# Kernel optimization log

Hardware: AMD Instinct MI355X
Metric: run time of the kernel (lower is better)

## Reference

```python
import jax, jax.numpy as jnp
import numpy as np

RADIUS = 1.0  # from init_kwargs
B = 8388608

def setup_inputs() -> dict:
    key = jax.random.key(0)
    k1, k2 = jax.random.split(key)
    x = jax.random.normal(k1, (B, 3), dtype=jnp.float32)
    center = jax.random.normal(k2, (B, 3), dtype=jnp.float32)
    return {"x": x, "center": center}

def reference(x, center):
    # Closed-form solution of: min ||z - x||^2  s.t. ||z - center||^2 <= r^2
    # z = x if inside the ball, else center + r * (x - center)/||x - center||
    d = x - center                                   # [B, 3]
    n = jnp.linalg.norm(d, axis=-1, keepdims=True)   # [B, 1]
    scale = jnp.minimum(jnp.float32(1.0), RADIUS / jnp.maximum(n, jnp.float32(1e-12)))
    return center + d * scale
```

## Files before the change

### kernel.cpp

```cpp
#include <hip/hip_runtime.h>


#define RADIUS 1.0f

typedef float fvec4 __attribute__((ext_vector_type(4)));

__global__ __launch_bounds__(256) void circle_proj_ilp8(
    const fvec4* __restrict__ xv,
    const fvec4* __restrict__ cv,
    fvec4* __restrict__ ov,
    int ngroups)
{
    int t = blockIdx.x * blockDim.x + threadIdx.x;
    if (t >= ngroups) return;
    long base = (long)t * 6;

    fvec4 xr[6], cr[6];
#pragma unroll
    for (int k = 0; k < 6; ++k) xr[k] = xv[base + k];
#pragma unroll
    for (int k = 0; k < 6; ++k) cr[k] = cv[base + k];

    float px[24], pc[24], po[24];
#pragma unroll
    for (int k = 0; k < 6; ++k) {
#pragma unroll
        for (int j = 0; j < 4; ++j) {
            px[4*k + j] = xr[k][j];
            pc[4*k + j] = cr[k][j];
        }
    }

#pragma unroll
    for (int p = 0; p < 8; ++p) {
        float dx = px[3*p + 0] - pc[3*p + 0];
        float dy = px[3*p + 1] - pc[3*p + 1];
        float dz = px[3*p + 2] - pc[3*p + 2];
        float n  = sqrtf(dx*dx + dy*dy + dz*dz);
        float scale = fminf(1.0f, RADIUS / fmaxf(n, 1e-12f));
        po[3*p + 0] = pc[3*p + 0] + dx * scale;
        po[3*p + 1] = pc[3*p + 1] + dy * scale;
        po[3*p + 2] = pc[3*p + 2] + dz * scale;
    }

#pragma unroll
    for (int k = 0; k < 6; ++k) {
        fvec4 o = {po[4*k+0], po[4*k+1], po[4*k+2], po[4*k+3]};
        ov[base + k] = o;
    }
}

extern "C" void kernel_launch(void* const* d_in, const int* in_sizes, int n_in,
                              void* d_out, int out_size, void* d_ws, size_t ws_size,
                              hipStream_t stream) {
    const float* x = (const float*)d_in[0];
    const float* c = (const float*)d_in[1];
    float* out = (float*)d_out;

    long total_floats = in_sizes[0];
    int ngroups = (int)(total_floats / 24);

    int block = 256;
    int grid = (ngroups + block - 1) / block;

    circle_proj_ilp8<<<grid, block, 0, stream>>>(
        (const fvec4*)x, (const fvec4*)c, (fvec4*)out, ngroups);
}
```

Measured before the change: 242.9 us.

## Process 4 points per group with grid-stride loop and register prefetch

```diff
diff --git a/kernel.cpp b/kernel.cpp
--- a/kernel.cpp
+++ b/kernel.cpp
@@ -5,34 +5,19 @@
 
 typedef float fvec4 __attribute__((ext_vector_type(4)));
 
-__global__ __launch_bounds__(256) void circle_proj_ilp8(
-    const fvec4* __restrict__ xv,
-    const fvec4* __restrict__ cv,
-    fvec4* __restrict__ ov,
-    int ngroups)
+__device__ __forceinline__ void project4(const fvec4 xr[3], const fvec4 cr[3], fvec4 o[3])
 {
-    int t = blockIdx.x * blockDim.x + threadIdx.x;
-    if (t >= ngroups) return;
-    long base = (long)t * 6;
-
-    fvec4 xr[6], cr[6];
+    float px[12], pc[12], po[12];
 #pragma unroll
-    for (int k = 0; k < 6; ++k) xr[k] = xv[base + k];
-#pragma unroll
-    for (int k = 0; k < 6; ++k) cr[k] = cv[base + k];
-
-    float px[24], pc[24], po[24];
-#pragma unroll
-    for (int k = 0; k < 6; ++k) {
+    for (int k = 0; k < 3; ++k) {
 #pragma unroll
         for (int j = 0; j < 4; ++j) {
             px[4*k + j] = xr[k][j];
             pc[4*k + j] = cr[k][j];
         }
     }
-
 #pragma unroll
-    for (int p = 0; p < 8; ++p) {
+    for (int p = 0; p < 4; ++p) {
         float dx = px[3*p + 0] - pc[3*p + 0];
         float dy = px[3*p + 1] - pc[3*p + 1];
         float dz = px[3*p + 2] - pc[3*p + 2];
@@ -42,11 +27,53 @@
         po[3*p + 1] = pc[3*p + 1] + dy * scale;
         po[3*p + 2] = pc[3*p + 2] + dz * scale;
     }
+#pragma unroll
+    for (int k = 0; k < 3; ++k)
+        o[k] = (fvec4){po[4*k+0], po[4*k+1], po[4*k+2], po[4*k+3]};
+}
+
+template <int G>
+__global__ __launch_bounds__(256) void circle_proj_pipe(
+    const fvec4* __restrict__ xv,
+    const fvec4* __restrict__ cv,
+    fvec4* __restrict__ ov,
+    int ngroups, int stride_groups)
+{
+    int t = blockIdx.x * blockDim.x + threadIdx.x;
+
+    fvec4 xr[3], cr[3];
+    long g0 = t;
+    if (g0 < ngroups) {
+        long b = g0 * 3;
+#pragma unroll
+        for (int k = 0; k < 3; ++k) { xr[k] = xv[b + k]; cr[k] = cv[b + k]; }
+    }
 
 #pragma unroll
-    for (int k = 0; k < 6; ++k) {
-        fvec4 o = {po[4*k+0], po[4*k+1], po[4*k+2], po[4*k+3]};
-        ov[base + k] = o;
+    for (int it = 0; it < G; ++it) {
+        long g  = (long)t + (long)it * stride_groups;
+        long gn = g + stride_groups;
+
+        fvec4 xn[3], cn[3];
+        bool have_next = (it + 1 < G) && (gn < ngroups);
+        if (have_next) {
+            long b = gn * 3;
+#pragma unroll
+            for (int k = 0; k < 3; ++k) { xn[k] = xv[b + k]; cn[k] = cv[b + k]; }
+        }
+
+        if (g < ngroups) {
+            fvec4 o[3];
+            project4(xr, cr, o);
+            long b = g * 3;
+#pragma unroll
+            for (int k = 0; k < 3; ++k) ov[b + k] = o[k];
+        }
+
+        if (have_next) {
+#pragma unroll
+            for (int k = 0; k < 3; ++k) { xr[k] = xn[k]; cr[k] = cn[k]; }
+        }
     }
 }
 
@@ -58,11 +85,12 @@
     float* out = (float*)d_out;
 
     long total_floats = in_sizes[0];
-    int ngroups = (int)(total_floats / 24);
+    int ngroups = (int)(total_floats / 12);
+    constexpr int G = 4;
+    int nthreads = (ngroups + G - 1) / G;
+    int block = 256;
+    int grid = (nthreads + block - 1) / block;
 
-    int block = 256;
-    int grid = (ngroups + block - 1) / block;
-
-    circle_proj_ilp8<<<grid, block, 0, stream>>>(
-        (const fvec4*)x, (const fvec4*)c, (fvec4*)out, ngroups);
+    circle_proj_pipe<G><<<grid, block, 0, stream>>>(
+        (const fvec4*)x, (const fvec4*)c, (fvec4*)out, ngroups, nthreads);
 }
```

After: 246.6 us. No clear change (+1.5%).
